# Performance work log

Hardware: AMD Instinct MI355X
Metric: run time of the kernel (lower is better)

## Reference

```python
import jax, jax.numpy as jnp
import numpy as np

EMBED = 1024
HEADS = 16
HEAD_DIM = EMBED // HEADS
FF = 4096
B, T = 2, 2048


def setup_inputs() -> dict:
    key = jax.random.key(0)
    ks = jax.random.split(key, 12)
    s = lambda k, shape, fan: jax.random.normal(k, shape, jnp.float32) * (1.0 / np.sqrt(fan))
    return {
        "x": jax.random.normal(ks[0], (B, T, EMBED), jnp.float32),
        "qkv_w": s(ks[1], (EMBED, 3 * EMBED), EMBED),
        "qkv_b": jnp.zeros((3 * EMBED,), jnp.float32),
        "out_w": s(ks[2], (EMBED, EMBED), EMBED),
        "out_b": jnp.zeros((EMBED,), jnp.float32),
        "ff_w1": s(ks[3], (EMBED, FF), EMBED),
        "ff_b1": jnp.zeros((FF,), jnp.float32),
        "ff_w2": s(ks[4], (FF, EMBED), FF),
        "ff_b2": jnp.zeros((EMBED,), jnp.float32),
        "ln1_g": jnp.ones((EMBED,), jnp.float32),
        "ln1_b": jnp.zeros((EMBED,), jnp.float32),
        "ln2_g": jnp.ones((EMBED,), jnp.float32),
        "ln2_b": jnp.zeros((EMBED,), jnp.float32),
    }


def _layer_norm(x, g, b, eps=1e-5):
    mu = jnp.mean(x, axis=-1, keepdims=True)
    var = jnp.var(x, axis=-1, keepdims=True)
    return (x - mu) * jax.lax.rsqrt(var + eps) * g + b


def _attention(x, qkv_w, qkv_b, out_w, out_b):
    Bv, Tv, C = x.shape
    qkv = x @ qkv_w + qkv_b                      # [B,T,3C]
    qkv = qkv.reshape(Bv, Tv, 3, HEADS, HEAD_DIM)
    q, k, v = qkv[:, :, 0], qkv[:, :, 1], qkv[:, :, 2]  # [B,T,H,D]
    scale = 1.0 / np.sqrt(HEAD_DIM)
    scores = jnp.einsum("bqhd,bkhd->bhqk", q, k) * scale  # [B,H,T,T]
    attn = jax.nn.softmax(scores, axis=-1)
    out = jnp.einsum("bhqk,bkhd->bqhd", attn, v).reshape(Bv, Tv, C)
    return out @ out_w + out_b


def _ffn(x, w1, b1, w2, b2):
    h = jax.nn.gelu(x @ w1 + b1, approximate=False)
    return h @ w2 + b2


def reference(x, qkv_w, qkv_b, out_w, out_b, ff_w1, ff_b1, ff_w2, ff_b2,
              ln1_g, ln1_b, ln2_g, ln2_b):
    x = x + _attention(_layer_norm(x, ln1_g, ln1_b), qkv_w, qkv_b, out_w, out_b)
    x = x + _ffn(_layer_norm(x, ln2_g, ln2_b), ff_w1, ff_b1, ff_w2, ff_b2)
    return x
```

## Files before the change

kernel.cpp:

```cpp
#include <hip/hip_runtime.h>

#define E     1024
#define HEADS 16
#define HD    64
#define FFD   4096
#define TT    2048
#define MMDIM 4096
#define NKV   1024
#define PO    (32 * 2048 * 64)

typedef __bf16 bf16x8 __attribute__((ext_vector_type(8)));
typedef float f32x4 __attribute__((ext_vector_type(4)));
typedef float f32x16 __attribute__((ext_vector_type(16)));
typedef unsigned short u16;
typedef unsigned u32;
typedef u16 ushort8 __attribute__((ext_vector_type(8)));
typedef u16 us4 __attribute__((ext_vector_type(4)));
typedef u32 u32x4 __attribute__((ext_vector_type(4)));

__device__ __forceinline__ u16 f2bf(float f) {
  unsigned u = __float_as_uint(f);
  u = (u + 0x7fffu + ((u >> 16) & 1u)) >> 16;
  return (u16)u;
}
__device__ __forceinline__ float bf2f(u16 u) {
  return __uint_as_float(((unsigned)u) << 16);
}
__device__ __forceinline__ u32 cvtpk(float a, float b) {
  u32 r;
  asm("v_cvt_pk_bf16_f32 %0, %1, %2" : "=v"(r) : "v"(a), "v"(b));
  return r;
}

__device__ __forceinline__ void gload_lds16(const void* g, void* l) {
  __builtin_amdgcn_global_load_lds((__attribute__((address_space(1))) void*)g,
                                   (__attribute__((address_space(3))) void*)l,
                                   16, 0, 0);
}

__global__ void __launch_bounds__(256) ln_kernel(const float* __restrict__ x,
                                                 const float* __restrict__ g,
                                                 const float* __restrict__ b,
                                                 u16* __restrict__ out) {
  int row = blockIdx.x;
  int t = threadIdx.x;
  const float4 v = reinterpret_cast<const float4*>(x + (size_t)row * E)[t];
  float s = v.x + v.y + v.z + v.w;
  float s2 = v.x * v.x + v.y * v.y + v.z * v.z + v.w * v.w;
#pragma unroll
  for (int m = 1; m < 64; m <<= 1) {
    s += __shfl_xor(s, m);
    s2 += __shfl_xor(s2, m);
  }
  __shared__ float red[8];
  int wave = t >> 6, lane = t & 63;
  if (lane == 0) { red[wave] = s; red[wave + 4] = s2; }
  __syncthreads();
  s = red[0] + red[1] + red[2] + red[3];
  s2 = red[4] + red[5] + red[6] + red[7];
  float mean = s * (1.f / E);
  float var = s2 * (1.f / E) - mean * mean;
  float inv = rsqrtf(var + 1e-5f);
  const float4 gv = reinterpret_cast<const float4*>(g)[t];
  const float4 bv = reinterpret_cast<const float4*>(b)[t];
  us4 pk;
  pk.x = f2bf((v.x - mean) * inv * gv.x + bv.x);
  pk.y = f2bf((v.y - mean) * inv * gv.y + bv.y);
  pk.z = f2bf((v.z - mean) * inv * gv.z + bv.z);
  pk.w = f2bf((v.w - mean) * inv * gv.w + bv.w);
  *(us4*)(out + (size_t)row * E + t * 4) = pk;
}

__global__ void __launch_bounds__(256) transpose4(const float* __restrict__ w0,
                                                  const float* __restrict__ w1,
                                                  const float* __restrict__ w2,
                                                  const float* __restrict__ w3,
                                                  u16* __restrict__ o0,
                                                  u16* __restrict__ o1,
                                                  u16* __restrict__ o2,
                                                  u16* __restrict__ o3) {
  __shared__ float tile[32][33];
  int b = blockIdx.x;
  const float* in;
  u16* out;
  int K, N, bx, by;
  if (b < 3072) {
    in = w0; out = o0; K = 1024; N = 3072; bx = b % 96; by = b / 96;
  } else if (b < 4096) {
    int r = b - 3072; in = w1; out = o1; K = 1024; N = 1024; bx = r % 32; by = r / 32;
  } else if (b < 8192) {
    int r = b - 4096; in = w2; out = o2; K = 1024; N = 4096; bx = r % 128; by = r / 128;
  } else {
    int r = b - 8192; in = w3; out = o3; K = 4096; N = 1024; bx = r % 32; by = r / 32;
  }
  int k0 = by * 32, n0 = bx * 32;
  int tx = threadIdx.x, ty = threadIdx.y;
#pragma unroll
  for (int i = ty; i < 32; i += 8)
    tile[i][tx] = in[(size_t)(k0 + i) * N + n0 + tx];
  __syncthreads();
#pragma unroll
  for (int i = ty; i < 32; i += 8)
    out[(size_t)(n0 + i) * K + k0 + tx] = f2bf(tile[tx][i]);
}

template <int MODE>
__global__ void __launch_bounds__(256) gemm2p(const u16* __restrict__ Aa,
                                              const u16* __restrict__ Bt,
                                              const float* __restrict__ bias,
                                              const float* __restrict__ resid,
                                              u16* __restrict__ ob0,
                                              u16* __restrict__ ob1,
                                              u16* __restrict__ ob2,
                                              float* __restrict__ of,
                                              int N, int K, int lda, int ldb) {
  __shared__ __align__(16) u16 As[2][128 * 64];
  __shared__ __align__(16) u16 Bs[2][128 * 64];
  const int nxy = gridDim.x * gridDim.y;
  const int lin = blockIdx.y * gridDim.x + blockIdx.x;
  const int g = (lin & 7) * (nxy >> 3) + (lin >> 3);
  const int s = g >> 6, o = g & 63;
  const int gx8 = gridDim.x >> 3;
  const int sx = s % gx8, sy = s / gx8;
  const int n0 = (sx * 8 + (o & 7)) * 128;
  const int m0 = (sy * 8 + (o >> 3)) * 128;
  const int tid = threadIdx.x, lane = tid & 63;
  const int wave = tid >> 6, wr = wave >> 1, wc = wave & 1;
  const int l15 = lane & 15, hi4 = lane >> 4, l7 = lane & 7;
  const size_t koff = (size_t)blockIdx.z * K;
  const int nt = K >> 6;

  f32x4 acc[4][4];
#pragma unroll
  for (int i = 0; i < 4; i++)
#pragma unroll
    for (int j = 0; j < 4; j++) acc[i][j] = (f32x4){0.f, 0.f, 0.f, 0.f};

  const u16* ApR[4];
  const u16* BpR[4];
#pragma unroll
  for (int r = 0; r < 4; r++) {
    int c = tid + r * 256;
    int row = c >> 3;
    int col = ((c & 7) ^ (row & 7)) * 8;
    ApR[r] = Aa + (size_t)(m0 + row) * lda + koff + col;
    BpR[r] = Bt + (size_t)(n0 + row) * ldb + koff + col;
  }

  const int xk0 = (hi4 << 4) ^ (l7 << 4);
  const int xk1 = (64 + (hi4 << 4)) ^ (l7 << 4);

#define STAGE2P(T, BUF)                                                        \
  do {                                                                         \
    int k0_ = (T) << 6;                                                        \
    _Pragma("unroll") for (int r_ = 0; r_ < 4; r_++) {                         \
      int c_ = tid + r_ * 256;                                                 \
      gload_lds16(ApR[r_] + k0_, &As[BUF][c_ * 8]);                            \
      gload_lds16(BpR[r_] + k0_, &Bs[BUF][c_ * 8]);                            \
    }                                                                          \
  } while (0)

  STAGE2P(0, 0);
  asm volatile("s_waitcnt vmcnt(0)" ::: "memory");
  __builtin_amdgcn_s_barrier();
  __builtin_amdgcn_sched_barrier(0);

  for (int t = 0; t < nt; ++t) {
    const int cur = t & 1;
    if (t + 1 < nt) {
      if (cur == 0) STAGE2P(t + 1, 1);
      else          STAGE2P(t + 1, 0);
    }
    const char* ab = (const char*)&As[0][0] + cur * 16384;
    const char* bb = (const char*)&Bs[0][0] + cur * 16384;
    bf16x8 a0[4], a1[4], b0[4], b1[4];
#pragma unroll
    for (int i = 0; i < 4; i++) {
      int rowb = (wr * 64 + i * 16 + l15) * 128;
      a0[i] = *(const bf16x8*)(ab + rowb + xk0);
      a1[i] = *(const bf16x8*)(ab + rowb + xk1);
    }
#pragma unroll
    for (int j = 0; j < 4; j++) {
      int rowb = (wc * 64 + j * 16 + l15) * 128;
      b0[j] = *(const bf16x8*)(bb + rowb + xk0);
      b1[j] = *(const bf16x8*)(bb + rowb + xk1);
    }
    asm volatile("s_waitcnt lgkmcnt(0)" ::: "memory");
    __builtin_amdgcn_sched_barrier(0);
    __builtin_amdgcn_s_setprio(1);
#pragma unroll
    for (int i = 0; i < 4; i++)
#pragma unroll
      for (int j = 0; j < 4; j++) {
        acc[i][j] = __builtin_amdgcn_mfma_f32_16x16x32_bf16(a0[i], b0[j], acc[i][j], 0, 0, 0);
        acc[i][j] = __builtin_amdgcn_mfma_f32_16x16x32_bf16(a1[i], b1[j], acc[i][j], 0, 0, 0);
      }
    __builtin_amdgcn_s_setprio(0);
    asm volatile("s_waitcnt vmcnt(0)" ::: "memory");
    __builtin_amdgcn_s_barrier();
    __builtin_amdgcn_sched_barrier(0);
  }
#undef STAGE2P

#pragma unroll
  for (int i = 0; i < 4; i++) {
#pragma unroll
    for (int j = 0; j < 4; j++) {
      int mb = m0 + wr * 64 + i * 16 + (hi4 << 2);
      int n = n0 + wc * 64 + j * 16 + l15;
      float bv = (MODE == 3) ? 0.f : bias[n];
      float v4[4];
#pragma unroll
      for (int r = 0; r < 4; r++) v4[r] = acc[i][j][r] + bv;
      if (MODE == 0) {
        int b_ = mb >> 11;
        int t = mb & 2047;
        int s_ = n >> 10;
        int hd = n & 1023;
        int h_ = hd >> 6;
        int d = hd & 63;
        size_t bh = (size_t)b_ * HEADS + h_;
        if (s_ == 0) {
#pragma unroll
          for (int r = 0; r < 4; r++)
            ob0[(bh * TT + (t + r)) * HD + d] = f2bf(v4[r] * 0.125f);
        } else if (s_ == 1) {
#pragma unroll
          for (int r = 0; r < 4; r++)
            ob1[(bh * TT + (t + r)) * HD + d] = f2bf(v4[r]);
        } else {
          us4 pk;
#pragma unroll
          for (int r = 0; r < 4; r++) pk[r] = f2bf(v4[r]);
          *(us4*)&ob2[(bh * HD + d) * TT + t] = pk;
        }
      } else if (MODE == 2) {
#pragma unroll
        for (int r = 0; r < 4; r++)
          ob0[(size_t)(mb + r) * FFD + n] =
              f2bf(0.5f * v4[r] * (1.f + erff(v4[r] * 0.70710678118f)));
      } else {
        if (blockIdx.z == 0) {
          float bz = bias[n];
#pragma unroll
          for (int r = 0; r < 4; r++) {
            size_t idx = (size_t)(mb + r) * E + n;
            of[idx] = v4[r] + bz + resid[idx];
          }
        } else {
#pragma unroll
          for (int r = 0; r < 4; r++)
            ob0[(size_t)(mb + r) * N + n] = f2bf(v4[r]);
        }
      }
    }
  }
}

__global__ void __launch_bounds__(256) addp_reduce(const u16* __restrict__ p1,
                                                   float* __restrict__ out) {
  size_t i = ((size_t)blockIdx.x * 256 + threadIdx.x) * 4;
  us4 a = *(const us4*)(p1 + i);
  float4 o = *(const float4*)(out + i);
  o.x += bf2f(a.x);
  o.y += bf2f(a.y);
  o.z += bf2f(a.z);
  o.w += bf2f(a.w);
  *(float4*)(out + i) = o;
}

__global__ void __launch_bounds__(512, 4) attn_kernel(const u16* __restrict__ Qb,
                                                      const u16* __restrict__ Kb,
                                                      const u16* __restrict__ Vt,
                                                      u16* __restrict__ op,
                                                      float2* __restrict__ ml) {
  __shared__ __align__(16) u16 Ks[2][64 * 64];
  __shared__ __align__(16) u16 Vs[2][64 * 64];
  const int bid = blockIdx.x;
  const int bh = bid & 31;
  const int qblk = (bid >> 5) & 7;
  const int part = bid >> 8;
  const int pstart = part * NKV;
  const int tid = threadIdx.x;
  const int w = tid >> 6, lane = tid & 63;
  const int lq = lane & 31, hi = lane >> 5;
  const int q0 = qblk * 256 + w * 32;

  const u16* Qp = Qb + ((size_t)bh * TT + q0 + lq) * HD + hi * 8;
  bf16x8 qf[4];
#pragma unroll
  for (int c = 0; c < 4; c++) qf[c] = *(const bf16x8*)(Qp + c * 16);

  const int srow = tid >> 3, schk = tid & 7;
  const u16* Kg = Kb + ((size_t)bh * TT + pstart + srow) * HD + ((schk ^ (srow & 7)) * 8);
  const u16* Vg = Vt + ((size_t)bh * HD + srow) * TT + pstart + ((schk ^ (srow & 7)) * 8);
  u16* kdst = &Ks[0][0] + tid * 8;
  u16* vdst = &Vs[0][0] + tid * 8;

  int ofs[8];
#pragma unroll
  for (int c = 0; c < 8; c++) ofs[c] = (c ^ (lq & 7)) << 4;

  f32x16 o0, o1;
#pragma unroll
  for (int r = 0; r < 16; r++) { o0[r] = 0.f; o1[r] = 0.f; }
  float m_run = -1e30f, l_run = 0.f;

#define STAGEKV(T, BUF)                                                        \
  do {                                                                         \
    gload_lds16(Kg + (size_t)(T) * 64 * HD, kdst + (BUF) * 4096);              \
    gload_lds16(Vg + (T) * 64, vdst + (BUF) * 4096);                           \
  } while (0)

  STAGEKV(0, 0);
  asm volatile("s_waitcnt vmcnt(0)" ::: "memory");
  __builtin_amdgcn_s_barrier();
  __builtin_amdgcn_sched_barrier(0);

  const int NT = NKV / 64;
  for (int t = 0; t < NT; ++t) {
    const int buf = t & 1;
    if (t + 1 < NT) STAGEKV(t + 1, buf ^ 1);
    const char* kT = (const char*)&Ks[buf][0];
    const char* vT = (const char*)&Vs[buf][0];
#pragma unroll
    for (int ss = 0; ss < 2; ++ss) {
      const char* kR = kT + (ss * 32 + lq) * 128;
      bf16x8 kf[4];
#pragma unroll
      for (int c = 0; c < 4; c++) kf[c] = *(const bf16x8*)(kR + ofs[c * 2 + hi]);
      const char* vR0 = vT + lq * 128;
      const char* vR1 = vT + (32 + lq) * 128;
      bf16x8 v00 = *(const bf16x8*)(vR0 + ofs[ss * 4 + 0 + hi]);
      bf16x8 v01 = *(const bf16x8*)(vR0 + ofs[ss * 4 + 2 + hi]);
      bf16x8 v10 = *(const bf16x8*)(vR1 + ofs[ss * 4 + 0 + hi]);
      bf16x8 v11 = *(const bf16x8*)(vR1 + ofs[ss * 4 + 2 + hi]);
      asm volatile("s_waitcnt lgkmcnt(0)" ::: "memory");
      __builtin_amdgcn_sched_barrier(0);

      f32x16 s;
#pragma unroll
      for (int r = 0; r < 16; r++) s[r] = 0.f;
      __builtin_amdgcn_s_setprio(1);
#pragma unroll
      for (int c = 0; c < 4; c++)
        s = __builtin_amdgcn_mfma_f32_32x32x16_bf16(kf[c], qf[c], s, 0, 0, 0);
      __builtin_amdgcn_s_setprio(0);

      float mx = s[0];
#pragma unroll
      for (int r = 1; r < 16; r++) mx = fmaxf(mx, s[r]);
      mx = fmaxf(mx, __shfl_xor(mx, 32));

      if (__any(mx > m_run + 8.f)) {
        float mn = fmaxf(m_run, mx);
        float al = __expf(m_run - mn);
#pragma unroll
        for (int r = 0; r < 16; r++) { o0[r] *= al; o1[r] *= al; }
        l_run *= al;
        m_run = mn;
      }

      float p[16], ps = 0.f;
#pragma unroll
      for (int r = 0; r < 16; r++) {
        p[r] = __expf(s[r] - m_run);
        ps += p[r];
      }
      l_run += ps + __shfl_xor(ps, 32);

      u32 wv[8];
#pragma unroll
      for (int c = 0; c < 2; c++) {
        u32 qA = cvtpk(p[c * 8 + 0], p[c * 8 + 1]);
        u32 qB = cvtpk(p[c * 8 + 2], p[c * 8 + 3]);
        u32 qC = cvtpk(p[c * 8 + 4], p[c * 8 + 5]);
        u32 qD = cvtpk(p[c * 8 + 6], p[c * 8 + 7]);
        u32 As_ = __shfl_xor(qA, 32), Bs_ = __shfl_xor(qB, 32);
        u32 Cs_ = __shfl_xor(qC, 32), Ds_ = __shfl_xor(qD, 32);
        wv[c * 4 + 0] = hi ? Cs_ : qA;
        wv[c * 4 + 1] = hi ? Ds_ : qB;
        wv[c * 4 + 2] = hi ? qC : As_;
        wv[c * 4 + 3] = hi ? qD : Bs_;
      }
      u32x4 t0 = {wv[0], wv[1], wv[2], wv[3]};
      u32x4 t1 = {wv[4], wv[5], wv[6], wv[7]};
      bf16x8 pf0 = __builtin_bit_cast(bf16x8, t0);
      bf16x8 pf1 = __builtin_bit_cast(bf16x8, t1);

      __builtin_amdgcn_s_setprio(1);
      o0 = __builtin_amdgcn_mfma_f32_32x32x16_bf16(v00, pf0, o0, 0, 0, 0);
      o0 = __builtin_amdgcn_mfma_f32_32x32x16_bf16(v01, pf1, o0, 0, 0, 0);
      o1 = __builtin_amdgcn_mfma_f32_32x32x16_bf16(v10, pf0, o1, 0, 0, 0);
      o1 = __builtin_amdgcn_mfma_f32_32x32x16_bf16(v11, pf1, o1, 0, 0, 0);
      __builtin_amdgcn_s_setprio(0);
    }
    asm volatile("s_waitcnt vmcnt(0)" ::: "memory");
    __builtin_amdgcn_s_barrier();
    __builtin_amdgcn_sched_barrier(0);
  }
#undef STAGEKV

  float rl = 1.f / l_run;
  u16* opP = op + (size_t)part * PO + ((size_t)bh * TT + q0 + lq) * HD;
#pragma unroll
  for (int r = 0; r < 16; r++) {
    int d = (r & 3) + ((r >> 2) << 3) + (hi << 2);
    opP[d] = f2bf(o0[r] * rl);
    opP[32 + d] = f2bf(o1[r] * rl);
  }
  if (hi == 0) {
    float2 v;
    v.x = m_run;
    v.y = l_run;
    ml[(size_t)part * (32 * TT) + bh * TT + q0 + lq] = v;
  }
}

__global__ void __launch_bounds__(256) attn_merge(const u16* __restrict__ op,
                                                  const float2* __restrict__ ml,
                                                  u16* __restrict__ O) {
  int idx = blockIdx.x * 256 + threadIdx.x;
  int bh = idx >> 14;
  int q = (idx >> 3) & 2047;
  int d0 = (idx & 7) * 8;
  int mli = bh * TT + q;
  float2 ab0 = ml[mli];
  float2 ab1 = ml[32 * TT + mli];
  float ms = fmaxf(ab0.x, ab1.x);
  float w0 = ab0.y * __expf(ab0.x - ms);
  float w1 = ab1.y * __expf(ab1.x - ms);
  float inv = 1.f / (w0 + w1);
  w0 *= inv;
  w1 *= inv;
  size_t base = ((size_t)bh * TT + q) * HD + d0;
  ushort8 a = *(const ushort8*)(op + base);
  ushort8 b = *(const ushort8*)(op + PO + base);
  ushort8 o;
#pragma unroll
  for (int k = 0; k < 8; k++) o[k] = f2bf(w0 * bf2f(a[k]) + w1 * bf2f(b[k]));
  size_t obase = ((size_t)(bh >> 4) * TT + q) * E + (bh & 15) * HD + d0;
  *(ushort8*)(O + obase) = o;
}

extern "C" void kernel_launch(void* const* d_in, const int* in_sizes, int n_in,
                              void* d_out, int out_size, void* d_ws, size_t ws_size,
                              hipStream_t stream) {
  (void)in_sizes; (void)n_in; (void)out_size; (void)ws_size;
  const float* x = (const float*)d_in[0];
  const float* qkv_w = (const float*)d_in[1];
  const float* qkv_b = (const float*)d_in[2];
  const float* out_w = (const float*)d_in[3];
  const float* out_b = (const float*)d_in[4];
  const float* ff_w1 = (const float*)d_in[5];
  const float* ff_b1 = (const float*)d_in[6];
  const float* ff_w2 = (const float*)d_in[7];
  const float* ff_b2 = (const float*)d_in[8];
  const float* ln1_g = (const float*)d_in[9];
  const float* ln1_b = (const float*)d_in[10];
  const float* ln2_g = (const float*)d_in[11];
  const float* ln2_b = (const float*)d_in[12];

  char* ws = (char*)d_ws;
  u16* outwt = (u16*)(ws + 0);
  u16* ffw1t = (u16*)(ws + 2097152);
  u16* ffw2t = (u16*)(ws + 10485760);
  u16* qkvwt = (u16*)(ws + 18874368);
  u16* ln_out = (u16*)(ws + 25165824);
  float* x1 = (float*)(ws + 33554432);
  u16* qb = (u16*)(ws + 50331648);
  u16* kb = (u16*)(ws + 58720256);
  u16* vt = (u16*)(ws + 67108864);
  u16* attn_o = (u16*)(ws + 75497472);
  u16* opbuf = (u16*)(ws + 18874368);
  float2* mlbuf = (float2*)(ws + 35651584);
  u16* hbuf = (u16*)(ws + 50331648);
  u16* pproj = (u16*)(ws + 18874368);
  u16* pbuf = (u16*)(ws + 0);

  transpose4<<<dim3(12288), dim3(32, 8), 0, stream>>>(
      qkv_w, out_w, ff_w1, ff_w2, qkvwt, outwt, ffw1t, ffw2t);

  ln_kernel<<<MMDIM, 256, 0, stream>>>(x, ln1_g, ln1_b, ln_out);
  gemm2p<0><<<dim3(3072 / 128, MMDIM / 128), 256, 0, stream>>>(
      ln_out, qkvwt, qkv_b, nullptr, qb, kb, vt, nullptr, 3072, 1024, 1024, 1024);
  attn_kernel<<<dim3(2 * 8 * 32), 512, 0, stream>>>(qb, kb, vt, opbuf, mlbuf);
  attn_merge<<<dim3(32 * TT * 8 / 256), 256, 0, stream>>>(opbuf, mlbuf, attn_o);
  gemm2p<3><<<dim3(1024 / 128, MMDIM / 128, 2), 256, 0, stream>>>(
      attn_o, outwt, out_b, x, pproj, nullptr, nullptr, x1, 1024, 512, 1024, 1024);
  addp_reduce<<<(size_t)MMDIM * E / 1024, 256, 0, stream>>>(pproj, x1);
  ln_kernel<<<MMDIM, 256, 0, stream>>>(x1, ln2_g, ln2_b, ln_out);
  gemm2p<2><<<dim3(4096 / 128, MMDIM / 128), 256, 0, stream>>>(
      ln_out, ffw1t, ff_b1, nullptr, hbuf, nullptr, nullptr, nullptr, 4096, 1024, 1024, 1024);
  gemm2p<3><<<dim3(1024 / 128, MMDIM / 128, 2), 256, 0, stream>>>(
      hbuf, ffw2t, ff_b2, x1, pbuf, nullptr, nullptr, (float*)d_out, 1024, 2048, 4096, 4096);
  addp_reduce<<<(size_t)MMDIM * E / 1024, 256, 0, stream>>>(pbuf, (float*)d_out);
}
```

Baseline: 261.0 us.

## Widen GEMM tiles to 128x256 with 8 waves and K-step 32

New measurement: 285.0 us. 9.2% more time.

```diff
diff --git a/kernel.cpp b/kernel.cpp
--- a/kernel.cpp
+++ b/kernel.cpp
@@ -105,30 +105,31 @@
 }
 
 template <int MODE>
-__global__ void __launch_bounds__(256) gemm2p(const u16* __restrict__ Aa,
-                                              const u16* __restrict__ Bt,
-                                              const float* __restrict__ bias,
-                                              const float* __restrict__ resid,
-                                              u16* __restrict__ ob0,
-                                              u16* __restrict__ ob1,
-                                              u16* __restrict__ ob2,
-                                              float* __restrict__ of,
-                                              int N, int K, int lda, int ldb) {
-  __shared__ __align__(16) u16 As[2][128 * 64];
-  __shared__ __align__(16) u16 Bs[2][128 * 64];
-  const int nxy = gridDim.x * gridDim.y;
-  const int lin = blockIdx.y * gridDim.x + blockIdx.x;
+__global__ void __launch_bounds__(512) gemm2pw(const u16* __restrict__ Aa,
+                                               const u16* __restrict__ Bt,
+                                               const float* __restrict__ bias,
+                                               const float* __restrict__ resid,
+                                               u16* __restrict__ ob0,
+                                               u16* __restrict__ ob1,
+                                               u16* __restrict__ ob2,
+                                               float* __restrict__ of,
+                                               int N, int K, int lda, int ldb) {
+  __shared__ __align__(16) u16 As[2][128 * 32];
+  __shared__ __align__(16) u16 Bs[2][256 * 32];
+  const int gx = gridDim.x;
+  const int nxy = gx * gridDim.y;
+  const int lin = blockIdx.y * gx + blockIdx.x;
   const int g = (lin & 7) * (nxy >> 3) + (lin >> 3);
-  const int s = g >> 6, o = g & 63;
-  const int gx8 = gridDim.x >> 3;
-  const int sx = s % gx8, sy = s / gx8;
-  const int n0 = (sx * 8 + (o & 7)) * 128;
-  const int m0 = (sy * 8 + (o >> 3)) * 128;
+  const int s = g >> 5, o = g & 31;
+  const int gx4 = gx >> 2;
+  const int sx = s % gx4, sy = s / gx4;
+  const int n0 = (sx * 4 + (o & 3)) * 256;
+  const int m0 = (sy * 8 + (o >> 2)) * 128;
   const int tid = threadIdx.x, lane = tid & 63;
-  const int wave = tid >> 6, wr = wave >> 1, wc = wave & 1;
-  const int l15 = lane & 15, hi4 = lane >> 4, l7 = lane & 7;
+  const int w = tid >> 6, wr = w >> 2, wc = w & 3;
+  const int l15 = lane & 15, hi4 = lane >> 4;
   const size_t koff = (size_t)blockIdx.z * K;
-  const int nt = K >> 6;
+  const int nt = K >> 5;
 
   f32x4 acc[4][4];
 #pragma unroll
@@ -136,31 +137,25 @@
 #pragma unroll
     for (int j = 0; j < 4; j++) acc[i][j] = (f32x4){0.f, 0.f, 0.f, 0.f};
 
-  const u16* ApR[4];
-  const u16* BpR[4];
-#pragma unroll
-  for (int r = 0; r < 4; r++) {
-    int c = tid + r * 256;
-    int row = c >> 3;
-    int col = ((c & 7) ^ (row & 7)) * 8;
-    ApR[r] = Aa + (size_t)(m0 + row) * lda + koff + col;
-    BpR[r] = Bt + (size_t)(n0 + row) * ldb + koff + col;
-  }
-
-  const int xk0 = (hi4 << 4) ^ (l7 << 4);
-  const int xk1 = (64 + (hi4 << 4)) ^ (l7 << 4);
-
-#define STAGE2P(T, BUF)                                                        \
+  const int arow = tid >> 2, aslot = tid & 3;
+  const int asw = (arow & 3) ^ ((arow >> 2) & 3);
+  const int brow1 = arow + 128;
+  const u16* Ap = Aa + (size_t)(m0 + arow) * lda + koff + (aslot ^ asw) * 8;
+  const u16* Bq0 = Bt + (size_t)(n0 + arow) * ldb + koff + (aslot ^ asw) * 8;
+  const u16* Bq1 = Bt + (size_t)(n0 + brow1) * ldb + koff + (aslot ^ asw) * 8;
+
+  const int rsw = (l15 & 3) ^ ((l15 >> 2) & 3);
+  const int rdofs = (hi4 ^ rsw) << 4;
+
+#define STAGEW(T, BUF)                                                         \
   do {                                                                         \
-    int k0_ = (T) << 6;                                                        \
-    _Pragma("unroll") for (int r_ = 0; r_ < 4; r_++) {                         \
-      int c_ = tid + r_ * 256;                                                 \
-      gload_lds16(ApR[r_] + k0_, &As[BUF][c_ * 8]);                            \
-      gload_lds16(BpR[r_] + k0_, &Bs[BUF][c_ * 8]);                            \
-    }                                                                          \
+    int k0_ = (T) << 5;                                                        \
+    gload_lds16(Ap + k0_, (char*)&As[BUF][0] + tid * 16);                      \
+    gload_lds16(Bq0 + k0_, (char*)&Bs[BUF][0] + tid * 16);                     \
+    gload_lds16(Bq1 + k0_, (char*)&Bs[BUF][0] + (tid + 512) * 16);             \
   } while (0)
 
-  STAGE2P(0, 0);
+  STAGEW(0, 0);
   asm volatile("s_waitcnt vmcnt(0)" ::: "memory");
   __builtin_amdgcn_s_barrier();
   __builtin_amdgcn_sched_barrier(0);
@@ -168,40 +163,32 @@
   for (int t = 0; t < nt; ++t) {
     const int cur = t & 1;
     if (t + 1 < nt) {
-      if (cur == 0) STAGE2P(t + 1, 1);
-      else          STAGE2P(t + 1, 0);
+      if (cur == 0) STAGEW(t + 1, 1);
+      else          STAGEW(t + 1, 0);
     }
-    const char* ab = (const char*)&As[0][0] + cur * 16384;
-    const char* bb = (const char*)&Bs[0][0] + cur * 16384;
-    bf16x8 a0[4], a1[4], b0[4], b1[4];
-#pragma unroll
-    for (int i = 0; i < 4; i++) {
-      int rowb = (wr * 64 + i * 16 + l15) * 128;
-      a0[i] = *(const bf16x8*)(ab + rowb + xk0);
-      a1[i] = *(const bf16x8*)(ab + rowb + xk1);
-    }
-#pragma unroll
-    for (int j = 0; j < 4; j++) {
-      int rowb = (wc * 64 + j * 16 + l15) * 128;
-      b0[j] = *(const bf16x8*)(bb + rowb + xk0);
-      b1[j] = *(const bf16x8*)(bb + rowb + xk1);
-    }
+    const char* ab = (const char*)&As[cur][0];
+    const char* bb = (const char*)&Bs[cur][0];
+    bf16x8 a[4], b[4];
+#pragma unroll
+    for (int i = 0; i < 4; i++)
+      a[i] = *(const bf16x8*)(ab + (wr * 64 + i * 16 + l15) * 64 + rdofs);
+#pragma unroll
+    for (int j = 0; j < 4; j++)
+      b[j] = *(const bf16x8*)(bb + (wc * 64 + j * 16 + l15) * 64 + rdofs);
     asm volatile("s_waitcnt lgkmcnt(0)" ::: "memory");
     __builtin_amdgcn_sched_barrier(0);
     __builtin_amdgcn_s_setprio(1);
 #pragma unroll
     for (int i = 0; i < 4; i++)
 #pragma unroll
-      for (int j = 0; j < 4; j++) {
-        acc[i][j] = __builtin_amdgcn_mfma_f32_16x16x32_bf16(a0[i], b0[j], acc[i][j], 0, 0, 0);
-        acc[i][j] = __builtin_amdgcn_mfma_f32_16x16x32_bf16(a1[i], b1[j], acc[i][j], 0, 0, 0);
-      }
+      for (int j = 0; j < 4; j++)
+        acc[i][j] = __builtin_amdgcn_mfma_f32_16x16x32_bf16(a[i], b[j], acc[i][j], 0, 0, 0);
     __builtin_amdgcn_s_setprio(0);
     asm volatile("s_waitcnt vmcnt(0)" ::: "memory");
     __builtin_amdgcn_s_barrier();
     __builtin_amdgcn_sched_barrier(0);
   }
-#undef STAGE2P
+#undef STAGEW
 
 #pragma unroll
   for (int i = 0; i < 4; i++) {
@@ -483,17 +470,17 @@
       qkv_w, out_w, ff_w1, ff_w2, qkvwt, outwt, ffw1t, ffw2t);
 
   ln_kernel<<<MMDIM, 256, 0, stream>>>(x, ln1_g, ln1_b, ln_out);
-  gemm2p<0><<<dim3(3072 / 128, MMDIM / 128), 256, 0, stream>>>(
+  gemm2pw<0><<<dim3(3072 / 256, MMDIM / 128), 512, 0, stream>>>(
       ln_out, qkvwt, qkv_b, nullptr, qb, kb, vt, nullptr, 3072, 1024, 1024, 1024);
   attn_kernel<<<dim3(2 * 8 * 32), 512, 0, stream>>>(qb, kb, vt, opbuf, mlbuf);
   attn_merge<<<dim3(32 * TT * 8 / 256), 256, 0, stream>>>(opbuf, mlbuf, attn_o);
-  gemm2p<3><<<dim3(1024 / 128, MMDIM / 128, 2), 256, 0, stream>>>(
+  gemm2pw<3><<<dim3(1024 / 256, MMDIM / 128, 2), 512, 0, stream>>>(
       attn_o, outwt, out_b, x, pproj, nullptr, nullptr, x1, 1024, 512, 1024, 1024);
   addp_reduce<<<(size_t)MMDIM * E / 1024, 256, 0, stream>>>(pproj, x1);
   ln_kernel<<<MMDIM, 256, 0, stream>>>(x1, ln2_g, ln2_b, ln_out);
-  gemm2p<2><<<dim3(4096 / 128, MMDIM / 128), 256, 0, stream>>>(
+  gemm2pw<2><<<dim3(4096 / 256, MMDIM / 128), 512, 0, stream>>>(
       ln_out, ffw1t, ff_b1, nullptr, hbuf, nullptr, nullptr, nullptr, 4096, 1024, 1024, 1024);
-  gemm2p<3><<<dim3(1024 / 128, MMDIM / 128, 2), 256, 0, stream>>>(
+  gemm2pw<3><<<dim3(1024 / 256, MMDIM / 128, 2), 512, 0, stream>>>(
       hbuf, ffw2t, ff_b2, x1, pbuf, nullptr, nullptr, (float*)d_out, 1024, 2048, 4096, 4096);
   addp_reduce<<<(size_t)MMDIM * E / 1024, 256, 0, stream>>>(pbuf, (float*)d_out);
 }
```

## Use wider 128x256 tile GEMM with 512 threads for QKV and FFN1

Applied to the files above, without the earlier changes.

New measurement: 251.4 us (median of 2 runs). -3.7%, faster.

```diff
diff --git a/kernel.cpp b/kernel.cpp
--- a/kernel.cpp
+++ b/kernel.cpp
@@ -105,13 +105,136 @@
 }
 
 template <int MODE>
+__global__ void __launch_bounds__(512) gemm2pw(const u16* __restrict__ Aa,
+                                               const u16* __restrict__ Bt,
+                                               const float* __restrict__ bias,
+                                               u16* __restrict__ ob0,
+                                               u16* __restrict__ ob1,
+                                               u16* __restrict__ ob2,
+                                               int N, int K, int lda, int ldb) {
+  __shared__ __align__(16) u16 As[2][128 * 32];
+  __shared__ __align__(16) u16 Bs[2][256 * 32];
+  const int gx = gridDim.x;
+  const int nxy = gx * gridDim.y;
+  const int lin = blockIdx.y * gx + blockIdx.x;
+  const int g = (lin & 7) * (nxy >> 3) + (lin >> 3);
+  const int s = g >> 5, o = g & 31;
+  const int gx4 = gx >> 2;
+  const int sx = s % gx4, sy = s / gx4;
+  const int n0 = (sx * 4 + (o & 3)) * 256;
+  const int m0 = (sy * 8 + (o >> 2)) * 128;
+  const int tid = threadIdx.x, lane = tid & 63;
+  const int w = tid >> 6, wr = w >> 2, wc = w & 3;
+  const int l15 = lane & 15, hi4 = lane >> 4;
+  const int nt = K >> 5;
+
+  f32x4 acc[4][4];
+#pragma unroll
+  for (int i = 0; i < 4; i++)
+#pragma unroll
+    for (int j = 0; j < 4; j++) acc[i][j] = (f32x4){0.f, 0.f, 0.f, 0.f};
+
+  const int arow = tid >> 2, aslot = tid & 3;
+  const int asw = (arow & 3) ^ ((arow >> 2) & 3);
+  const int brow1 = arow + 128;
+  const u16* Ap = Aa + (size_t)(m0 + arow) * lda + (aslot ^ asw) * 8;
+  const u16* Bq0 = Bt + (size_t)(n0 + arow) * ldb + (aslot ^ asw) * 8;
+  const u16* Bq1 = Bt + (size_t)(n0 + brow1) * ldb + (aslot ^ asw) * 8;
+
+  const int rsw = (l15 & 3) ^ ((l15 >> 2) & 3);
+  const int rdofs = (hi4 ^ rsw) << 4;
+
+#define STAGEW(T, BUF)                                                         \
+  do {                                                                         \
+    int k0_ = (T) << 5;                                                        \
+    gload_lds16(Ap + k0_, (char*)&As[BUF][0] + tid * 16);                      \
+    gload_lds16(Bq0 + k0_, (char*)&Bs[BUF][0] + tid * 16);                     \
+    gload_lds16(Bq1 + k0_, (char*)&Bs[BUF][0] + (tid + 512) * 16);             \
+  } while (0)
+
+  STAGEW(0, 0);
+  asm volatile("s_waitcnt vmcnt(0)" ::: "memory");
+  __builtin_amdgcn_s_barrier();
+  __builtin_amdgcn_sched_barrier(0);
+
+  for (int t = 0; t < nt; ++t) {
+    const int cur = t & 1;
+    if (t + 1 < nt) {
+      if (cur == 0) STAGEW(t + 1, 1);
+      else          STAGEW(t + 1, 0);
+    }
+    const char* ab = (const char*)&As[cur][0];
+    const char* bb = (const char*)&Bs[cur][0];
+    bf16x8 a[4], b[4];
+#pragma unroll
+    for (int i = 0; i < 4; i++)
+      a[i] = *(const bf16x8*)(ab + (wr * 64 + i * 16 + l15) * 64 + rdofs);
+#pragma unroll
+    for (int j = 0; j < 4; j++)
+      b[j] = *(const bf16x8*)(bb + (wc * 64 + j * 16 + l15) * 64 + rdofs);
+    asm volatile("s_waitcnt lgkmcnt(0)" ::: "memory");
+    __builtin_amdgcn_sched_barrier(0);
+    __builtin_amdgcn_s_setprio(1);
+#pragma unroll
+    for (int i = 0; i < 4; i++)
+#pragma unroll
+      for (int j = 0; j < 4; j++)
+        acc[i][j] = __builtin_amdgcn_mfma_f32_16x16x32_bf16(a[i], b[j], acc[i][j], 0, 0, 0);
+    __builtin_amdgcn_s_setprio(0);
+    asm volatile("s_waitcnt vmcnt(0)" ::: "memory");
+    __builtin_amdgcn_s_barrier();
+    __builtin_amdgcn_sched_barrier(0);
+  }
+#undef STAGEW
+
+#pragma unroll
+  for (int i = 0; i < 4; i++) {
+#pragma unroll
+    for (int j = 0; j < 4; j++) {
+      int mb = m0 + wr * 64 + i * 16 + (hi4 << 2);
+      int n = n0 + wc * 64 + j * 16 + l15;
+      float bv = bias[n];
+      float v4[4];
+#pragma unroll
+      for (int r = 0; r < 4; r++) v4[r] = acc[i][j][r] + bv;
+      if (MODE == 0) {
+        int b_ = mb >> 11;
+        int t = mb & 2047;
+        int s_ = n >> 10;
+        int hd = n & 1023;
+        int h_ = hd >> 6;
+        int d = hd & 63;
+        size_t bh = (size_t)b_ * HEADS + h_;
+        if (s_ == 0) {
+#pragma unroll
+          for (int r = 0; r < 4; r++)
+            ob0[(bh * TT + (t + r)) * HD + d] = f2bf(v4[r] * 0.125f);
+        } else if (s_ == 1) {
+#pragma unroll
+          for (int r = 0; r < 4; r++)
+            ob1[(bh * TT + (t + r)) * HD + d] = f2bf(v4[r]);
+        } else {
+          us4 pk;
+#pragma unroll
+          for (int r = 0; r < 4; r++) pk[r] = f2bf(v4[r]);
+          *(us4*)&ob2[(bh * HD + d) * TT + t] = pk;
+        }
+      } else {
+#pragma unroll
+        for (int r = 0; r < 4; r++)
+          ob0[(size_t)(mb + r) * FFD + n] =
+              f2bf(0.5f * v4[r] * (1.f + erff(v4[r] * 0.70710678118f)));
+      }
+    }
+  }
+}
+
+template <int MODE>
 __global__ void __launch_bounds__(256) gemm2p(const u16* __restrict__ Aa,
                                               const u16* __restrict__ Bt,
                                               const float* __restrict__ bias,
                                               const float* __restrict__ resid,
                                               u16* __restrict__ ob0,
-                                              u16* __restrict__ ob1,
-                                              u16* __restrict__ ob2,
                                               float* __restrict__ of,
                                               int N, int K, int lda, int ldb) {
   __shared__ __align__(16) u16 As[2][128 * 64];
@@ -209,49 +332,18 @@
     for (int j = 0; j < 4; j++) {
       int mb = m0 + wr * 64 + i * 16 + (hi4 << 2);
       int n = n0 + wc * 64 + j * 16 + l15;
-      float bv = (MODE == 3) ? 0.f : bias[n];
-      float v4[4];
-#pragma unroll
-      for (int r = 0; r < 4; r++) v4[r] = acc[i][j][r] + bv;
-      if (MODE == 0) {
-        int b_ = mb >> 11;
-        int t = mb & 2047;
-        int s_ = n >> 10;
-        int hd = n & 1023;
-        int h_ = hd >> 6;
-        int d = hd & 63;
-        size_t bh = (size_t)b_ * HEADS + h_;
-        if (s_ == 0) {
-#pragma unroll
-          for (int r = 0; r < 4; r++)
-            ob0[(bh * TT + (t + r)) * HD + d] = f2bf(v4[r] * 0.125f);
-        } else if (s_ == 1) {
-#pragma unroll
-          for (int r = 0; r < 4; r++)
-            ob1[(bh * TT + (t + r)) * HD + d] = f2bf(v4[r]);
-        } else {
-          us4 pk;
-#pragma unroll
-          for (int r = 0; r < 4; r++) pk[r] = f2bf(v4[r]);
-          *(us4*)&ob2[(bh * HD + d) * TT + t] = pk;
-        }
-      } else if (MODE == 2) {
-#pragma unroll
-        for (int r = 0; r < 4; r++)
-          ob0[(size_t)(mb + r) * FFD + n] =
-              f2bf(0.5f * v4[r] * (1.f + erff(v4[r] * 0.70710678118f)));
-      } else {
+      if (MODE == 3) {
         if (blockIdx.z == 0) {
           float bz = bias[n];
 #pragma unroll
           for (int r = 0; r < 4; r++) {
             size_t idx = (size_t)(mb + r) * E + n;
-            of[idx] = v4[r] + bz + resid[idx];
+            of[idx] = acc[i][j][r] + bz + resid[idx];
           }
         } else {
 #pragma unroll
           for (int r = 0; r < 4; r++)
-            ob0[(size_t)(mb + r) * N + n] = f2bf(v4[r]);
+            ob0[(size_t)(mb + r) * N + n] = f2bf(acc[i][j][r]);
         }
       }
     }
@@ -483,17 +575,17 @@
       qkv_w, out_w, ff_w1, ff_w2, qkvwt, outwt, ffw1t, ffw2t);
 
   ln_kernel<<<MMDIM, 256, 0, stream>>>(x, ln1_g, ln1_b, ln_out);
-  gemm2p<0><<<dim3(3072 / 128, MMDIM / 128), 256, 0, stream>>>(
-      ln_out, qkvwt, qkv_b, nullptr, qb, kb, vt, nullptr, 3072, 1024, 1024, 1024);
+  gemm2pw<0><<<dim3(3072 / 256, MMDIM / 128), 512, 0, stream>>>(
+      ln_out, qkvwt, qkv_b, qb, kb, vt, 3072, 1024, 1024, 1024);
   attn_kernel<<<dim3(2 * 8 * 32), 512, 0, stream>>>(qb, kb, vt, opbuf, mlbuf);
   attn_merge<<<dim3(32 * TT * 8 / 256), 256, 0, stream>>>(opbuf, mlbuf, attn_o);
   gemm2p<3><<<dim3(1024 / 128, MMDIM / 128, 2), 256, 0, stream>>>(
-      attn_o, outwt, out_b, x, pproj, nullptr, nullptr, x1, 1024, 512, 1024, 1024);
+      attn_o, outwt, out_b, x, pproj, x1, 1024, 512, 1024, 1024);
   addp_reduce<<<(size_t)MMDIM * E / 1024, 256, 0, stream>>>(pproj, x1);
   ln_kernel<<<MMDIM, 256, 0, stream>>>(x1, ln2_g, ln2_b, ln_out);
-  gemm2p<2><<<dim3(4096 / 128, MMDIM / 128), 256, 0, stream>>>(
-      ln_out, ffw1t, ff_b1, nullptr, hbuf, nullptr, nullptr, nullptr, 4096, 1024, 1024, 1024);
+  gemm2pw<2><<<dim3(4096 / 256, MMDIM / 128), 512, 0, stream>>>(
+      ln_out, ffw1t, ff_b1, hbuf, nullptr, nullptr, 4096, 1024, 1024, 1024);
   gemm2p<3><<<dim3(1024 / 128, MMDIM / 128, 2), 256, 0, stream>>>(
-      hbuf, ffw2t, ff_b2, x1, pbuf, nullptr, nullptr, (float*)d_out, 1024, 2048, 4096, 4096);
+      hbuf, ffw2t, ff_b2, x1, pbuf, (float*)d_out, 1024, 2048, 4096, 4096);
   addp_reduce<<<(size_t)MMDIM * E / 1024, 256, 0, stream>>>(pbuf, (float*)d_out);
 }
```
